# Optimization experiments

Hardware: AMD Instinct MI355X
Metric: run time of the kernel (lower is better)

## Reference

```python
import jax, jax.numpy as jnp
import numpy as np

B, T, D = 2, 2048, 512
H = 8
DH = D // H
DECAY = 0.99
SCALE = DH ** -0.5
NEG = -1e30

_J6 = jnp.array([[0, 0, 0, 0, 0, 1], [0, 0, 0, 0, -1, 0], [0, 0, 0, 1, 0, 0],
                 [0, 0, 1, 0, 0, 0], [0, -1, 0, 0, 0, 0], [1, 0, 0, 0, 0, 0]],
                dtype=jnp.float32)
_PAIRS4 = [(0, 1), (0, 2), (0, 3), (1, 2), (1, 3), (2, 3)]


def exterior(p1, p2):
    # p1, p2: [..., 4] -> normalized Plucker line coords [..., 6]
    parts = [p1[..., i] * p2[..., j] - p1[..., j] * p2[..., i] for i, j in _PAIRS4]
    L = jnp.stack(parts, axis=-1)
    n = jnp.sqrt(jnp.sum(L * L, axis=-1, keepdims=True))
    return L / jnp.maximum(n, 1e-12)


def setup_inputs() -> dict:
    key = jax.random.key(0)
    ks = jax.random.split(key, 16)
    s = 0.02
    return {
        "x": jax.random.normal(ks[0], (B, T, D), jnp.float32),
        "qkv_w": jax.random.normal(ks[1], (3 * D, D), jnp.float32) * s,
        "qkv_b": jnp.zeros((3 * D,), jnp.float32),
        "w1_write": jax.random.normal(ks[2], (4 * H, D), jnp.float32) * s,
        "w2_write": jax.random.normal(ks[3], (4 * H, D), jnp.float32) * s,
        "w1_read": jax.random.normal(ks[4], (4 * H, D), jnp.float32) * s,
        "w2_read": jax.random.normal(ks[5], (4 * H, D), jnp.float32) * s,
        "mem_value_w": jax.random.normal(ks[6], (D, D), jnp.float32) * s,
        "mem_value_b": jnp.zeros((D,), jnp.float32),
        "mem_gate_w": jax.random.normal(ks[7], (H, D), jnp.float32) * s,
        "mem_gate_b": jnp.zeros((H,), jnp.float32),
        "mem_scale": jnp.full((H,), 0.1, jnp.float32),
        "out_w": jax.random.normal(ks[8], (D, D), jnp.float32) * s,
        "out_b": jnp.zeros((D,), jnp.float32),
    }


def reference(x, qkv_w, qkv_b, w1_write, w2_write, w1_read, w2_read,
              mem_value_w, mem_value_b, mem_gate_w, mem_gate_b, mem_scale,
              out_w, out_b):
    b, t, d = x.shape
    # --- standard causal attention (dropout in eval mode = identity) ---
    qkv = (x @ qkv_w.T + qkv_b).reshape(b, t, 3, H, DH)
    qkv = jnp.transpose(qkv, (2, 0, 3, 1, 4))  # [3,B,H,T,dh]
    q, k, v = qkv[0], qkv[1], qkv[2]
    scores = jnp.einsum('bhtd,bhsd->bhts', q, k) * SCALE
    i = jnp.arange(t)
    upper = i[:, None] < i[None, :]  # strictly upper -> masked
    scores = jnp.where(upper, NEG, scores)
    attn = jax.nn.softmax(scores, axis=-1)
    seq_out = jnp.einsum('bhts,bhsd->bhtd', attn, v)
    seq_out = jnp.transpose(seq_out, (0, 2, 1, 3)).reshape(b, t, d)
    # --- exterior-algebra Gram memory ---
    x_prev = jnp.concatenate([jnp.zeros((b, 1, d), x.dtype), x[:, :-1]], axis=1)
    w1 = (x_prev @ w1_write.T).reshape(b, t, H, 4)
    w2 = (x @ w2_write.T).reshape(b, t, H, 4)
    write_lines = exterior(w1, w2)  # [B,T,H,6]
    r1 = (x @ w1_read.T).reshape(b, t, H, 4)
    r2 = (x @ w2_read.T).reshape(b, t, H, 4)
    read_lines = exterior(r1, r2)  # [B,T,H,6]
    J_write = jnp.einsum('bthi,ij->bthj', write_lines, _J6)
    # incidence[b,h,i,j] = <read_i, J write_j>
    incidence = jnp.einsum('bihk,bjhk->bhij', read_lines, J_write)  # [B,H,T,T]
    # decay weights, strictly lower triangular (j < i); also acts as causal mask
    pos = jnp.arange(t, dtype=x.dtype)
    delta = pos[:, None] - pos[None, :]
    weights = jnp.where(delta > 0, jnp.power(jnp.asarray(DECAY, x.dtype), delta), 0.0)
    mem_score = jnp.sum((incidence * incidence) * weights[None, None], axis=-1)  # [B,H,T]
    # --- gating ---
    mem_val = x @ mem_value_w.T + mem_value_b  # [B,T,D]
    gate = jax.nn.sigmoid(x @ mem_gate_w.T + mem_gate_b)  # [B,T,H]
    mem_score_t = jnp.transpose(mem_score, (0, 2, 1))  # [B,T,H]
    gated = jax.nn.sigmoid(mem_score_t * mem_scale[None, None, :]) * gate
    gated = jnp.mean(gated, axis=-1, keepdims=True)  # [B,T,1]
    return (seq_out + gated * mem_val) @ out_w.T + out_b
```

## Files before the change

kernel.cpp:

```cpp
#include <hip/hip_runtime.h>
#include <math.h>

#define B_ 2
#define T_ 2048
#define D_ 512
#define H_ 8
#define DH_ 64
#define SCALE_ 0.125f
#define DECAY_ 0.99f

static constexpr size_t QSZ = (size_t)B_ * H_ * T_ * DH_;

typedef __bf16 bf16x8 __attribute__((ext_vector_type(8)));
typedef float f32x4 __attribute__((ext_vector_type(4)));

__device__ inline ushort f2bf(float f) {
  uint u = __float_as_uint(f);
  u += 0x7FFF + ((u >> 16) & 1);
  return (ushort)(u >> 16);
}

__device__ inline float bf2f(ushort v) {
  return __uint_as_float(((uint)v) << 16);
}

__device__ __forceinline__ void gload16(const ushort* g, ushort* l) {
  __builtin_amdgcn_global_load_lds(
      (const __attribute__((address_space(1))) void*)g,
      (__attribute__((address_space(3))) void*)l, 16, 0, 0);
}

__global__ __launch_bounds__(256) void cast_bf16_kernel(
    const float* __restrict__ x, const float* __restrict__ qkvw,
    const float* __restrict__ mvw, const float* __restrict__ ow,
    const float* __restrict__ w1w, const float* __restrict__ w2w,
    const float* __restrict__ w1r, const float* __restrict__ w2r,
    const float* __restrict__ mgw, ushort* __restrict__ dst)
{
  size_t e0 = ((size_t)blockIdx.x * 256 + threadIdx.x) * 8;
  const float* src = nullptr;
  if (e0 < 2097152)      src = x + e0;
  else if (e0 < 2883584) src = qkvw + (e0 - 2097152);
  else if (e0 < 3145728) src = mvw + (e0 - 2883584);
  else if (e0 < 3276800) {
    size_t off = e0 - 3145728;
    int row = (int)(off >> 9), col = (int)(off & 511);
    if (row < 32)       src = w1w + (size_t)row * 512 + col;
    else if (row < 64)  src = w2w + (size_t)(row - 32) * 512 + col;
    else if (row < 96)  src = w1r + (size_t)(row - 64) * 512 + col;
    else if (row < 128) src = w2r + (size_t)(row - 96) * 512 + col;
    else if (row < 136) src = mgw + (size_t)(row - 128) * 512 + col;
    else src = nullptr;
  } else if (e0 < 3538944) src = ow + (e0 - 3276800);
  ushort tmp[8];
  if (src) {
    float4 a = *(const float4*)(src);
    float4 b = *(const float4*)(src + 4);
    tmp[0] = f2bf(a.x); tmp[1] = f2bf(a.y); tmp[2] = f2bf(a.z); tmp[3] = f2bf(a.w);
    tmp[4] = f2bf(b.x); tmp[5] = f2bf(b.y); tmp[6] = f2bf(b.z); tmp[7] = f2bf(b.w);
  } else {
#pragma unroll
    for (int i = 0; i < 8; i++) tmp[i] = 0;
  }
  *(uint4*)(dst + e0) = *(uint4*)tmp;
}

template<int EPI>
__global__ __launch_bounds__(256) void mfma_gemm(const ushort* __restrict__ A,
    const ushort* __restrict__ W, const float* __restrict__ bias,
    const float* __restrict__ bias2, void* __restrict__ Cout,
    ushort* __restrict__ memval16, float* __restrict__ proj, int M, int N, int K)
{
  __shared__ __align__(16) ushort As[128 * 64];
  __shared__ __align__(16) ushort Ws[64 * 64];
  const int tid = threadIdx.x;
  const int wave = tid >> 6, lane = tid & 63;
  const int col16 = lane & 15, grp = lane >> 4;
  const int wr = wave >> 1, wc = wave & 1;
  const int gx = gridDim.x;
  const int nwg = gx * gridDim.y;
  const int p = blockIdx.y * gx + blockIdx.x;
  const int wg = (p & 7) * (nwg >> 3) + (p >> 3);
  const int bm = (wg / gx) * 128, bn = (wg % gx) * 64;

  f32x4 acc[4][2] = {};
  const int lrow = lane >> 3, lcol = (lane & 7) * 8;

  for (int k0 = 0; k0 < K; k0 += 64) {
    __syncthreads();
#pragma unroll
    for (int i = 0; i < 4; i++) {
      int q = i * 4 + wave;
      gload16(A + (size_t)(bm + q * 8 + lrow) * K + k0 + lcol, &As[q * 512]);
    }
#pragma unroll
    for (int i = 0; i < 2; i++) {
      int q = i * 4 + wave;
      gload16(W + (size_t)(bn + q * 8 + lrow) * K + k0 + lcol, &Ws[q * 512]);
    }
    __syncthreads();
#pragma unroll
    for (int kk = 0; kk < 2; kk++) {
      bf16x8 a[4], b[2];
#pragma unroll
      for (int m = 0; m < 4; m++)
        a[m] = *(const bf16x8*)&As[(wr * 64 + m * 16 + col16) * 64 + kk * 32 + grp * 8];
#pragma unroll
      for (int n = 0; n < 2; n++)
        b[n] = *(const bf16x8*)&Ws[(wc * 32 + n * 16 + col16) * 64 + kk * 32 + grp * 8];
#pragma unroll
      for (int m = 0; m < 4; m++)
#pragma unroll
        for (int n = 0; n < 2; n++)
          acc[m][n] = __builtin_amdgcn_mfma_f32_16x16x32_bf16(a[m], b[n], acc[m][n], 0, 0, 0);
    }
  }

  if (EPI == 1) {
    ushort* q16 = (ushort*)Cout;
    ushort* k16 = q16 + QSZ;
    ushort* vt  = q16 + 2 * QSZ;
    const int sec = bn >> 9;
    if (sec == 2) {
#pragma unroll
      for (int n = 0; n < 2; n++) {
        int col = bn + wc * 32 + n * 16 + col16;
        float bv = bias[col];
        int h = (col >> 6) & 7, dh = col & 63;
#pragma unroll
        for (int m = 0; m < 4; m++) {
          int row0 = bm + wr * 64 + m * 16 + grp * 4;
          int b = row0 >> 11, t0 = row0 & 2047;
          ushort tmp4[4];
#pragma unroll
          for (int r = 0; r < 4; r++) tmp4[r] = f2bf(acc[m][n][r] + bv);
          *(uint2*)(vt + ((size_t)(b * H_ + h) * 64 + dh) * T_ + t0) = *(uint2*)tmp4;
        }
      }
    } else {
#pragma unroll
      for (int n = 0; n < 2; n++) {
        int col = bn + wc * 32 + n * 16 + col16;
        float bv;
        if (sec < 2)       bv = bias[col];
        else if (sec == 3) bv = bias2[col - 1536];
        else               bv = 0.f;
        int h = (col >> 6) & 7, dh = col & 63;
#pragma unroll
        for (int m = 0; m < 4; m++) {
#pragma unroll
          for (int r = 0; r < 4; r++) {
            int row = bm + wr * 64 + m * 16 + grp * 4 + r;
            int b = row >> 11, t = row & 2047;
            float val = acc[m][n][r] + bv;
            size_t bh = (size_t)(b * H_ + h);
            if (sec == 0)      q16[(bh * T_ + t) * 64 + dh] = f2bf(val * (SCALE_ * 1.44269504f));
            else if (sec == 1) k16[(bh * T_ + t) * 64 + dh] = f2bf(val);
            else if (sec == 3) memval16[(size_t)row * 512 + (col - 1536)] = f2bf(val);
            else               proj[(size_t)row * 256 + (col - 2048)] = val;
          }
        }
      }
    }
  } else {
    float* C = (float*)Cout;
#pragma unroll
    for (int n = 0; n < 2; n++) {
      int col = bn + wc * 32 + n * 16 + col16;
      float bv = bias[col];
#pragma unroll
      for (int m = 0; m < 4; m++) {
#pragma unroll
        for (int r = 0; r < 4; r++) {
          int row = bm + wr * 64 + m * 16 + grp * 4 + r;
          C[(size_t)row * N + col] = acc[m][n][r] + bv;
        }
      }
    }
  }
}

__global__ __launch_bounds__(256) void lines_kernel(
    const float* __restrict__ proj, const float* __restrict__ gb,
    float* __restrict__ u_out, float* __restrict__ r_out, float* __restrict__ gate_out)
{
  int gid = blockIdx.x * 256 + threadIdx.x;
  int bt = gid >> 3, h = gid & 7;
  int b = bt >> 11, t = bt & 2047;
  const float* pr = proj + (size_t)bt * 256;
  const int pi[6] = {0, 0, 0, 1, 1, 2};
  const int pj[6] = {1, 2, 3, 2, 3, 3};
  float p1[4], p2[4];
#pragma unroll
  for (int e = 0; e < 4; e++) {
    p1[e] = (t == 0) ? 0.f : proj[(size_t)(bt - 1) * 256 + h * 4 + e];
    p2[e] = pr[32 + h * 4 + e];
  }
  float L[6], n2 = 0.f;
#pragma unroll
  for (int e = 0; e < 6; e++) {
    L[e] = p1[pi[e]] * p2[pj[e]] - p1[pj[e]] * p2[pi[e]];
    n2 = fmaf(L[e], L[e], n2);
  }
  float inv = 1.f / fmaxf(sqrtf(n2), 1e-12f);
  size_t base = (((size_t)(b * H_ + h)) * T_ + t) * 6;
  u_out[base + 0] =  L[5] * inv;
  u_out[base + 1] = -L[4] * inv;
  u_out[base + 2] =  L[3] * inv;
  u_out[base + 3] =  L[2] * inv;
  u_out[base + 4] = -L[1] * inv;
  u_out[base + 5] =  L[0] * inv;
#pragma unroll
  for (int e = 0; e < 4; e++) {
    p1[e] = pr[64 + h * 4 + e];
    p2[e] = pr[96 + h * 4 + e];
  }
  n2 = 0.f;
#pragma unroll
  for (int e = 0; e < 6; e++) {
    L[e] = p1[pi[e]] * p2[pj[e]] - p1[pj[e]] * p2[pi[e]];
    n2 = fmaf(L[e], L[e], n2);
  }
  inv = 1.f / fmaxf(sqrtf(n2), 1e-12f);
#pragma unroll
  for (int e = 0; e < 6; e++) r_out[base + e] = L[e] * inv;
  gate_out[(size_t)bt * H_ + h] = 1.f / (1.f + __expf(-(pr[128 + h] + gb[h])));
}

__global__ __launch_bounds__(256) void attn_split32_kernel(
    const ushort* __restrict__ q16, const ushort* __restrict__ k16,
    const ushort* __restrict__ vt16, float* __restrict__ seq_out)
{
  const int blk = blockIdx.x;
  const int bh = blk & 15;
  const int rg = 63 - (blk >> 4);
  const int tid = threadIdx.x;
  const int w = tid >> 6, lane = tid & 63;
  const int col16 = lane & 15, grp = lane >> 4;

  __shared__ __align__(16) float smem[7680];
  ushort (*ps_)[32][72] = (ushort (*)[32][72])smem;
  float (*comb)[64][40] = (float (*)[64][40])smem;

  const int i0 = rg * 32;
  const ushort* qp0 = q16 + ((size_t)bh * T_ + i0 + col16) * 64 + grp * 8;
  bf16x8 aq[2][2];
  aq[0][0] = *(const bf16x8*)(qp0);
  aq[0][1] = *(const bf16x8*)(qp0 + 32);
  aq[1][0] = *(const bf16x8*)(qp0 + 16 * 64);
  aq[1][1] = *(const bf16x8*)(qp0 + 16 * 64 + 32);

  f32x4 o[2][4] = {};
  float lsum[2][4] = {};

  const ushort* kb = k16 + (size_t)bh * T_ * 64;
  const ushort* vb = vt16 + (size_t)bh * 64 * T_;

  const int ntiles = (rg >> 1) + 1;
  for (int kt = w; kt < ntiles; kt += 4) {
    const int j0 = kt * 64;
    bf16x8 vfrag[2][4];
#pragma unroll
    for (int ks2 = 0; ks2 < 2; ks2++)
#pragma unroll
      for (int n = 0; n < 4; n++)
        vfrag[ks2][n] = *(const bf16x8*)(vb + (size_t)(n * 16 + col16) * T_ +
                                         j0 + ks2 * 32 + grp * 8);
    f32x4 facc[2][4] = {};
#pragma unroll
    for (int jt = 0; jt < 4; jt++) {
      const ushort* kp = kb + (size_t)(j0 + jt * 16 + col16) * 64 + grp * 8;
      bf16x8 b0 = *(const bf16x8*)kp;
      bf16x8 b1 = *(const bf16x8*)(kp + 32);
#pragma unroll
      for (int rr = 0; rr < 2; rr++) {
        facc[rr][jt] = __builtin_amdgcn_mfma_f32_16x16x32_bf16(aq[rr][0], b0, facc[rr][jt], 0, 0, 0);
        facc[rr][jt] = __builtin_amdgcn_mfma_f32_16x16x32_bf16(aq[rr][1], b1, facc[rr][jt], 0, 0, 0);
      }
    }
    const bool lastt = (kt == ntiles - 1);
#pragma unroll
    for (int rr = 0; rr < 2; rr++)
#pragma unroll
      for (int jt = 0; jt < 4; jt++) {
        int j = j0 + jt * 16 + col16;
#pragma unroll
        for (int r = 0; r < 4; r++) {
          int i = i0 + rr * 16 + grp * 4 + r;
          float pv = (lastt && j > i) ? 0.f : exp2f(facc[rr][jt][r]);
          lsum[rr][r] += pv;
          ps_[w][rr * 16 + grp * 4 + r][jt * 16 + col16] = f2bf(pv);
        }
      }
#pragma unroll
    for (int ks2 = 0; ks2 < 2; ks2++)
#pragma unroll
      for (int rr = 0; rr < 2; rr++) {
        bf16x8 a = *(const bf16x8*)&ps_[w][rr * 16 + col16][ks2 * 32 + grp * 8];
#pragma unroll
        for (int n = 0; n < 4; n++)
          o[rr][n] = __builtin_amdgcn_mfma_f32_16x16x32_bf16(a, vfrag[ks2][n], o[rr][n], 0, 0, 0);
      }
  }

  __syncthreads();
  if (w > 0) {
    float* dst = &comb[w - 1][lane][0];
#pragma unroll
    for (int rr = 0; rr < 2; rr++)
#pragma unroll
      for (int n = 0; n < 4; n++)
        *(float4*)&dst[(rr * 4 + n) * 4] = *(float4*)&o[rr][n];
    *(float4*)&dst[32] = make_float4(lsum[0][0], lsum[0][1], lsum[0][2], lsum[0][3]);
    *(float4*)&dst[36] = make_float4(lsum[1][0], lsum[1][1], lsum[1][2], lsum[1][3]);
  }
  __syncthreads();
  if (w == 0) {
#pragma unroll
    for (int ww = 0; ww < 3; ww++) {
      const float* src = &comb[ww][lane][0];
#pragma unroll
      for (int rr = 0; rr < 2; rr++)
#pragma unroll
        for (int n = 0; n < 4; n++) {
          float4 v = *(const float4*)&src[(rr * 4 + n) * 4];
          o[rr][n][0] += v.x; o[rr][n][1] += v.y; o[rr][n][2] += v.z; o[rr][n][3] += v.w;
        }
      float4 l0 = *(const float4*)&src[32];
      float4 l1 = *(const float4*)&src[36];
      lsum[0][0] += l0.x; lsum[0][1] += l0.y; lsum[0][2] += l0.z; lsum[0][3] += l0.w;
      lsum[1][0] += l1.x; lsum[1][1] += l1.y; lsum[1][2] += l1.z; lsum[1][3] += l1.w;
    }
#pragma unroll
    for (int rr = 0; rr < 2; rr++)
#pragma unroll
      for (int r = 0; r < 4; r++) {
        float s = lsum[rr][r];
#pragma unroll
        for (int s2 = 1; s2 < 16; s2 <<= 1) s += __shfl_xor(s, s2);
        lsum[rr][r] = s;
      }
    const int b = bh >> 3, h = bh & 7;
#pragma unroll
    for (int rr = 0; rr < 2; rr++)
#pragma unroll
      for (int r = 0; r < 4; r++) {
        float inv = 1.f / lsum[rr][r];
        int i = i0 + rr * 16 + grp * 4 + r;
        float* op = seq_out + ((size_t)(b * T_) + i) * D_ + h * 64;
#pragma unroll
        for (int n = 0; n < 4; n++)
          op[n * 16 + col16] = o[rr][n][r] * inv;
      }
  }
}

__global__ __launch_bounds__(128) void memscore3_kernel(
    const float* __restrict__ u, const float* __restrict__ r, float* __restrict__ score)
{
  const int bh = blockIdx.x;
  const int c = blockIdx.y;
  const int tid = threadIdx.x;
  const int base = c << 7;
  const int jmax = base + 128;
  __shared__ float us_t[6][2048];
  __shared__ float red[128][25];

  const float* ug = u + (size_t)bh * T_ * 6;
  for (int idx = tid; idx < jmax * 6; idx += 128) {
    int j = idx / 6;
    int cmp = idx - j * 6;
    us_t[cmp][j] = ug[idx];
  }
  __syncthreads();

  float g[21];
#pragma unroll
  for (int q2 = 0; q2 < 21; q2++) g[q2] = 0.f;
  if (c > 0) {
    float w = __powf(DECAY_, (float)(128 - tid));
    const float d128 = 0.27624712f;
    for (int j = base - 128 + tid; j >= 0; j -= 128) {
      float u0 = us_t[0][j], u1 = us_t[1][j], u2 = us_t[2][j];
      float u3 = us_t[3][j], u4 = us_t[4][j], u5 = us_t[5][j];
      float w0 = w * u0, w1 = w * u1, w2 = w * u2, w3 = w * u3, w4 = w * u4;
      g[0] = fmaf(w0, u0, g[0]);  g[1] = fmaf(w0, u1, g[1]);
      g[2] = fmaf(w0, u2, g[2]);  g[3] = fmaf(w0, u3, g[3]);
      g[4] = fmaf(w0, u4, g[4]);  g[5] = fmaf(w0, u5, g[5]);
      g[6] = fmaf(w1, u1, g[6]);  g[7] = fmaf(w1, u2, g[7]);
      g[8] = fmaf(w1, u3, g[8]);  g[9] = fmaf(w1, u4, g[9]);
      g[10] = fmaf(w1, u5, g[10]); g[11] = fmaf(w2, u2, g[11]);
      g[12] = fmaf(w2, u3, g[12]); g[13] = fmaf(w2, u4, g[13]);
      g[14] = fmaf(w2, u5, g[14]); g[15] = fmaf(w3, u3, g[15]);
      g[16] = fmaf(w3, u4, g[16]); g[17] = fmaf(w3, u5, g[17]);
      g[18] = fmaf(w4, u4, g[18]); g[19] = fmaf(w4, u5, g[19]);
      g[20] = fmaf(w * u5, u5, g[20]);
      w *= d128;
    }
  }
#pragma unroll
  for (int q2 = 0; q2 < 21; q2++) red[tid][q2] = g[q2];
  __syncthreads();
  for (int off = 64; off > 0; off >>= 1) {
    if (tid < off) {
#pragma unroll
      for (int q2 = 0; q2 < 21; q2++) red[tid][q2] += red[tid + off][q2];
    }
    __syncthreads();
  }
  float M21[21];
#pragma unroll
  for (int q2 = 0; q2 < 21; q2++) M21[q2] = red[0][q2];

  const int i = base + tid;
  const float* ri = r + ((size_t)bh * T_ + i) * 6;
  float r0 = ri[0], r1 = ri[1], r2 = ri[2], r3 = ri[3], r4 = ri[4], r5 = ri[5];
  float q = M21[0] * r0 * r0 + M21[6] * r1 * r1 + M21[11] * r2 * r2
          + M21[15] * r3 * r3 + M21[18] * r4 * r4 + M21[20] * r5 * r5
          + 2.f * (M21[1] * r0 * r1 + M21[2] * r0 * r2 + M21[3] * r0 * r3
                 + M21[4] * r0 * r4 + M21[5] * r0 * r5 + M21[7] * r1 * r2
                 + M21[8] * r1 * r3 + M21[9] * r1 * r4 + M21[10] * r1 * r5
                 + M21[12] * r2 * r3 + M21[13] * r2 * r4 + M21[14] * r2 * r5
                 + M21[16] * r3 * r4 + M21[17] * r3 * r5 + M21[19] * r4 * r5);
  float wl = __powf(DECAY_, (float)tid);
  float sum = q * wl;
  float w = wl;
  const float invd = 1.0f / DECAY_;
  const int sbound = tid | 63;
  for (int s = 0; s < sbound; ++s) {
    float d = r0 * us_t[0][base + s] + r1 * us_t[1][base + s]
            + r2 * us_t[2][base + s] + r3 * us_t[3][base + s]
            + r4 * us_t[4][base + s] + r5 * us_t[5][base + s];
    if (s < tid) sum = fmaf(w, d * d, sum);
    w *= invd;
  }
  score[(size_t)bh * T_ + i] = sum;
}

__global__ __launch_bounds__(256) void gate_combine_kernel(
    const float* __restrict__ score, const float* __restrict__ gate,
    const float* __restrict__ mem_scale, const ushort* __restrict__ memval16,
    const float* __restrict__ seqo, ushort* __restrict__ seqo16)
{
  int bt = blockIdx.x;
  int b = bt / T_, t = bt % T_;
  __shared__ float g;
  if (threadIdx.x == 0) {
    float acc = 0.f;
#pragma unroll
    for (int h = 0; h < H_; h++) {
      float ms = score[((size_t)(b * H_ + h)) * T_ + t];
      float sg = 1.f / (1.f + __expf(-ms * mem_scale[h]));
      acc += sg * gate[(size_t)(b * T_ + t) * H_ + h];
    }
    g = acc * (1.0f / H_);
  }
  __syncthreads();
  float gv = g;
  size_t base = (size_t)(b * T_ + t) * D_;
  for (int d = threadIdx.x; d < D_; d += 256)
    seqo16[base + d] = f2bf(fmaf(gv, bf2f(memval16[base + d]), seqo[base + d]));
}

extern "C" void kernel_launch(void* const* d_in, const int* in_sizes, int n_in,
                              void* d_out, int out_size, void* d_ws, size_t ws_size,
                              hipStream_t stream) {
  const float* x     = (const float*)d_in[0];
  const float* qkvw  = (const float*)d_in[1];
  const float* qkvb  = (const float*)d_in[2];
  const float* w1w   = (const float*)d_in[3];
  const float* w2w   = (const float*)d_in[4];
  const float* w1r   = (const float*)d_in[5];
  const float* w2r   = (const float*)d_in[6];
  const float* mvw   = (const float*)d_in[7];
  const float* mvb   = (const float*)d_in[8];
  const float* mgw   = (const float*)d_in[9];
  const float* mgb   = (const float*)d_in[10];
  const float* mscl  = (const float*)d_in[11];
  const float* ow    = (const float*)d_in[12];
  const float* ob    = (const float*)d_in[13];
  (void)in_sizes; (void)n_in; (void)out_size; (void)ws_size;

  float* f = (float*)d_ws;
  float* seqo     = f;
  ushort* memval16 = (ushort*)(seqo + 2097152);
  float* proj     = (float*)(memval16 + 2097152);
  float* ul       = proj + 1048576;
  float* rl       = ul + 196608;
  float* gatep    = rl + 196608;
  float* msc      = gatep + 32768;
  ushort* x16    = (ushort*)(msc + 32768);
  ushort* wbig16 = x16 + 2097152;
  ushort* ow16   = wbig16 + 1179648;
  ushort* q16    = ow16 + 262144;
  ushort* k16    = q16 + QSZ;
  ushort* vt16   = k16 + QSZ;
  ushort* seqo16 = x16;

  const int M = B_ * T_;

  cast_bf16_kernel<<<dim3(1728), 256, 0, stream>>>(x, qkvw, mvw, ow,
                                                   w1w, w2w, w1r, w2r, mgw, x16);
  mfma_gemm<1><<<dim3(36, 32), 256, 0, stream>>>(x16, wbig16, qkvb, mvb, q16,
                                                 memval16, proj, M, 2304, D_);
  lines_kernel<<<dim3(128), 256, 0, stream>>>(proj, mgb, ul, rl, gatep);
  attn_split32_kernel<<<dim3(16 * 64), 256, 0, stream>>>(q16, k16, vt16, seqo);
  memscore3_kernel<<<dim3(16, 16), 128, 0, stream>>>(ul, rl, msc);
  gate_combine_kernel<<<dim3(B_ * T_), 256, 0, stream>>>(msc, gatep, mscl, memval16,
                                                         seqo, seqo16);
  mfma_gemm<0><<<dim3(8, 32), 256, 0, stream>>>(seqo16, ow16, ob, nullptr, d_out,
                                                nullptr, nullptr, M, D_, D_);
}
```

Measured before the change: 118.8 us.

## Fuse gating combine into attention epilogue and stage V tiles in LDS asynchronously

The separate gate_combine pass is split: a tiny gfac kernel computes the per-token gate factor, and the attention kernel's epilogue applies it with memval and writes the bf16 input for the output GEMM directly. This drops the fp32 seq_out round trip and one full-size elementwise kernel. Attention also now prefetches V tiles into swizzled LDS with asynchronous global-to-LDS loads (gload16) and overlaps the next tile's load with compute, instead of loading V fragments directly into registers. The cost is more LDS per block and a reordered launch sequence, in which memscore now has to finish before attention starts.

```diff
diff --git a/kernel.cpp b/kernel.cpp
--- a/kernel.cpp
+++ b/kernel.cpp
@@ -227,134 +227,6 @@
   gate_out[(size_t)bt * H_ + h] = 1.f / (1.f + __expf(-(pr[128 + h] + gb[h])));
 }
 
-__global__ __launch_bounds__(256) void attn_split32_kernel(
-    const ushort* __restrict__ q16, const ushort* __restrict__ k16,
-    const ushort* __restrict__ vt16, float* __restrict__ seq_out)
-{
-  const int blk = blockIdx.x;
-  const int bh = blk & 15;
-  const int rg = 63 - (blk >> 4);
-  const int tid = threadIdx.x;
-  const int w = tid >> 6, lane = tid & 63;
-  const int col16 = lane & 15, grp = lane >> 4;
-
-  __shared__ __align__(16) float smem[7680];
-  ushort (*ps_)[32][72] = (ushort (*)[32][72])smem;
-  float (*comb)[64][40] = (float (*)[64][40])smem;
-
-  const int i0 = rg * 32;
-  const ushort* qp0 = q16 + ((size_t)bh * T_ + i0 + col16) * 64 + grp * 8;
-  bf16x8 aq[2][2];
-  aq[0][0] = *(const bf16x8*)(qp0);
-  aq[0][1] = *(const bf16x8*)(qp0 + 32);
-  aq[1][0] = *(const bf16x8*)(qp0 + 16 * 64);
-  aq[1][1] = *(const bf16x8*)(qp0 + 16 * 64 + 32);
-
-  f32x4 o[2][4] = {};
-  float lsum[2][4] = {};
-
-  const ushort* kb = k16 + (size_t)bh * T_ * 64;
-  const ushort* vb = vt16 + (size_t)bh * 64 * T_;
-
-  const int ntiles = (rg >> 1) + 1;
-  for (int kt = w; kt < ntiles; kt += 4) {
-    const int j0 = kt * 64;
-    bf16x8 vfrag[2][4];
-#pragma unroll
-    for (int ks2 = 0; ks2 < 2; ks2++)
-#pragma unroll
-      for (int n = 0; n < 4; n++)
-        vfrag[ks2][n] = *(const bf16x8*)(vb + (size_t)(n * 16 + col16) * T_ +
-                                         j0 + ks2 * 32 + grp * 8);
-    f32x4 facc[2][4] = {};
-#pragma unroll
-    for (int jt = 0; jt < 4; jt++) {
-      const ushort* kp = kb + (size_t)(j0 + jt * 16 + col16) * 64 + grp * 8;
-      bf16x8 b0 = *(const bf16x8*)kp;
-      bf16x8 b1 = *(const bf16x8*)(kp + 32);
-#pragma unroll
-      for (int rr = 0; rr < 2; rr++) {
-        facc[rr][jt] = __builtin_amdgcn_mfma_f32_16x16x32_bf16(aq[rr][0], b0, facc[rr][jt], 0, 0, 0);
-        facc[rr][jt] = __builtin_amdgcn_mfma_f32_16x16x32_bf16(aq[rr][1], b1, facc[rr][jt], 0, 0, 0);
-      }
-    }
-    const bool lastt = (kt == ntiles - 1);
-#pragma unroll
-    for (int rr = 0; rr < 2; rr++)
-#pragma unroll
-      for (int jt = 0; jt < 4; jt++) {
-        int j = j0 + jt * 16 + col16;
-#pragma unroll
-        for (int r = 0; r < 4; r++) {
-          int i = i0 + rr * 16 + grp * 4 + r;
-          float pv = (lastt && j > i) ? 0.f : exp2f(facc[rr][jt][r]);
-          lsum[rr][r] += pv;
-          ps_[w][rr * 16 + grp * 4 + r][jt * 16 + col16] = f2bf(pv);
-        }
-      }
-#pragma unroll
-    for (int ks2 = 0; ks2 < 2; ks2++)
-#pragma unroll
-      for (int rr = 0; rr < 2; rr++) {
-        bf16x8 a = *(const bf16x8*)&ps_[w][rr * 16 + col16][ks2 * 32 + grp * 8];
-#pragma unroll
-        for (int n = 0; n < 4; n++)
-          o[rr][n] = __builtin_amdgcn_mfma_f32_16x16x32_bf16(a, vfrag[ks2][n], o[rr][n], 0, 0, 0);
-      }
-  }
-
-  __syncthreads();
-  if (w > 0) {
-    float* dst = &comb[w - 1][lane][0];
-#pragma unroll
-    for (int rr = 0; rr < 2; rr++)
-#pragma unroll
-      for (int n = 0; n < 4; n++)
-        *(float4*)&dst[(rr * 4 + n) * 4] = *(float4*)&o[rr][n];
-    *(float4*)&dst[32] = make_float4(lsum[0][0], lsum[0][1], lsum[0][2], lsum[0][3]);
-    *(float4*)&dst[36] = make_float4(lsum[1][0], lsum[1][1], lsum[1][2], lsum[1][3]);
-  }
-  __syncthreads();
-  if (w == 0) {
-#pragma unroll
-    for (int ww = 0; ww < 3; ww++) {
-      const float* src = &comb[ww][lane][0];
-#pragma unroll
-      for (int rr = 0; rr < 2; rr++)
-#pragma unroll
-        for (int n = 0; n < 4; n++) {
-          float4 v = *(const float4*)&src[(rr * 4 + n) * 4];
-          o[rr][n][0] += v.x; o[rr][n][1] += v.y; o[rr][n][2] += v.z; o[rr][n][3] += v.w;
-        }
-      float4 l0 = *(const float4*)&src[32];
-      float4 l1 = *(const float4*)&src[36];
-      lsum[0][0] += l0.x; lsum[0][1] += l0.y; lsum[0][2] += l0.z; lsum[0][3] += l0.w;
-      lsum[1][0] += l1.x; lsum[1][1] += l1.y; lsum[1][2] += l1.z; lsum[1][3] += l1.w;
-    }
-#pragma unroll
-    for (int rr = 0; rr < 2; rr++)
-#pragma unroll
-      for (int r = 0; r < 4; r++) {
-        float s = lsum[rr][r];
-#pragma unroll
-        for (int s2 = 1; s2 < 16; s2 <<= 1) s += __shfl_xor(s, s2);
-        lsum[rr][r] = s;
-      }
-    const int b = bh >> 3, h = bh & 7;
-#pragma unroll
-    for (int rr = 0; rr < 2; rr++)
-#pragma unroll
-      for (int r = 0; r < 4; r++) {
-        float inv = 1.f / lsum[rr][r];
-        int i = i0 + rr * 16 + grp * 4 + r;
-        float* op = seq_out + ((size_t)(b * T_) + i) * D_ + h * 64;
-#pragma unroll
-        for (int n = 0; n < 4; n++)
-          op[n * 16 + col16] = o[rr][n][r] * inv;
-      }
-  }
-}
-
 __global__ __launch_bounds__(128) void memscore3_kernel(
     const float* __restrict__ u, const float* __restrict__ r, float* __restrict__ score)
 {
@@ -437,29 +309,168 @@
   score[(size_t)bh * T_ + i] = sum;
 }
 
-__global__ __launch_bounds__(256) void gate_combine_kernel(
+__global__ __launch_bounds__(256) void gfac_kernel(
     const float* __restrict__ score, const float* __restrict__ gate,
-    const float* __restrict__ mem_scale, const ushort* __restrict__ memval16,
-    const float* __restrict__ seqo, ushort* __restrict__ seqo16)
+    const float* __restrict__ mem_scale, float* __restrict__ gfac)
 {
-  int bt = blockIdx.x;
-  int b = bt / T_, t = bt % T_;
-  __shared__ float g;
-  if (threadIdx.x == 0) {
-    float acc = 0.f;
-#pragma unroll
-    for (int h = 0; h < H_; h++) {
-      float ms = score[((size_t)(b * H_ + h)) * T_ + t];
-      float sg = 1.f / (1.f + __expf(-ms * mem_scale[h]));
-      acc += sg * gate[(size_t)(b * T_ + t) * H_ + h];
-    }
-    g = acc * (1.0f / H_);
-  }
+  int bt = blockIdx.x * 256 + threadIdx.x;
+  int b = bt >> 11, t = bt & 2047;
+  float acc = 0.f;
+#pragma unroll
+  for (int h = 0; h < H_; h++) {
+    float ms = score[((size_t)(b * H_ + h)) * T_ + t];
+    float sg = 1.f / (1.f + __expf(-ms * mem_scale[h]));
+    acc += sg * gate[(size_t)bt * H_ + h];
+  }
+  gfac[bt] = acc * (1.0f / H_);
+}
+
+__global__ __launch_bounds__(256) void attn_v3_kernel(
+    const ushort* __restrict__ q16, const ushort* __restrict__ k16,
+    const ushort* __restrict__ vt16, const ushort* __restrict__ memval16,
+    const float* __restrict__ gfac, ushort* __restrict__ seqo16)
+{
+  const int blk = blockIdx.x;
+  const int bh = blk & 15;
+  const int rg = 63 - (blk >> 4);
+  const int tid = threadIdx.x;
+  const int w = tid >> 6, lane = tid & 63;
+  const int col16 = lane & 15, grp = lane >> 4;
+
+  __shared__ __align__(16) ushort smemU[25600];
+  ushort* vt_lds = &smemU[w * 4096];
+  ushort* ps_w   = &smemU[16384 + w * 32 * 72];
+  float*  combf  = (float*)smemU;
+
+  const int i0 = rg * 32;
+  const ushort* qp0 = q16 + ((size_t)bh * T_ + i0 + col16) * 64 + grp * 8;
+  bf16x8 aq[2][2];
+  aq[0][0] = *(const bf16x8*)(qp0);
+  aq[0][1] = *(const bf16x8*)(qp0 + 32);
+  aq[1][0] = *(const bf16x8*)(qp0 + 16 * 64);
+  aq[1][1] = *(const bf16x8*)(qp0 + 16 * 64 + 32);
+
+  f32x4 o[2][4] = {};
+  float lsum[2][4] = {};
+
+  const ushort* kb = k16 + (size_t)bh * T_ * 64;
+  const ushort* vb = vt16 + (size_t)bh * 64 * T_;
+  const int vrow = lane >> 3;
+  const int vchk = ((lane & 7) ^ vrow) << 3;
+
+  const int ntiles = (rg >> 1) + 1;
+  if (w < ntiles) {
+    const int j0 = w * 64;
+#pragma unroll
+    for (int g = 0; g < 8; g++)
+      gload16(vb + (size_t)(g * 8 + vrow) * T_ + j0 + vchk, vt_lds + g * 512);
+  }
+
+  for (int kt = w; kt < ntiles; kt += 4) {
+    const int j0 = kt * 64;
+    f32x4 facc[2][4] = {};
+#pragma unroll
+    for (int jt = 0; jt < 4; jt++) {
+      const ushort* kp = kb + (size_t)(j0 + jt * 16 + col16) * 64 + grp * 8;
+      bf16x8 b0 = *(const bf16x8*)kp;
+      bf16x8 b1 = *(const bf16x8*)(kp + 32);
+#pragma unroll
+      for (int rr = 0; rr < 2; rr++) {
+        facc[rr][jt] = __builtin_amdgcn_mfma_f32_16x16x32_bf16(aq[rr][0], b0, facc[rr][jt], 0, 0, 0);
+        facc[rr][jt] = __builtin_amdgcn_mfma_f32_16x16x32_bf16(aq[rr][1], b1, facc[rr][jt], 0, 0, 0);
+      }
+    }
+    const bool lastt = (kt == ntiles - 1);
+#pragma unroll
+    for (int rr = 0; rr < 2; rr++)
+#pragma unroll
+      for (int jt = 0; jt < 4; jt++) {
+        int j = j0 + jt * 16 + col16;
+#pragma unroll
+        for (int r = 0; r < 4; r++) {
+          int i = i0 + rr * 16 + grp * 4 + r;
+          float pv = (lastt && j > i) ? 0.f : exp2f(facc[rr][jt][r]);
+          lsum[rr][r] += pv;
+          ps_w[(rr * 16 + grp * 4 + r) * 72 + jt * 16 + col16] = f2bf(pv);
+        }
+      }
+    asm volatile("s_waitcnt vmcnt(0)" ::: "memory");
+#pragma unroll
+    for (int ks2 = 0; ks2 < 2; ks2++)
+#pragma unroll
+      for (int rr = 0; rr < 2; rr++) {
+        bf16x8 a = *(const bf16x8*)&ps_w[(rr * 16 + col16) * 72 + ks2 * 32 + grp * 8];
+#pragma unroll
+        for (int n = 0; n < 4; n++) {
+          int d = n * 16 + col16;
+          int cs = (ks2 * 4 + grp) ^ (col16 & 7);
+          bf16x8 bv = *(const bf16x8*)&vt_lds[d * 64 + cs * 8];
+          o[rr][n] = __builtin_amdgcn_mfma_f32_16x16x32_bf16(a, bv, o[rr][n], 0, 0, 0);
+        }
+      }
+    __builtin_amdgcn_sched_barrier(0);
+    if (kt + 4 < ntiles) {
+      const int jn = (kt + 4) * 64;
+#pragma unroll
+      for (int g = 0; g < 8; g++)
+        gload16(vb + (size_t)(g * 8 + vrow) * T_ + jn + vchk, vt_lds + g * 512);
+    }
+  }
+
   __syncthreads();
-  float gv = g;
-  size_t base = (size_t)(b * T_ + t) * D_;
-  for (int d = threadIdx.x; d < D_; d += 256)
-    seqo16[base + d] = f2bf(fmaf(gv, bf2f(memval16[base + d]), seqo[base + d]));
+  if (w > 0) {
+    float* dst = &combf[((w - 1) * 64 + lane) * 40];
+#pragma unroll
+    for (int rr = 0; rr < 2; rr++)
+#pragma unroll
+      for (int n = 0; n < 4; n++)
+        *(float4*)&dst[(rr * 4 + n) * 4] = *(float4*)&o[rr][n];
+    *(float4*)&dst[32] = make_float4(lsum[0][0], lsum[0][1], lsum[0][2], lsum[0][3]);
+    *(float4*)&dst[36] = make_float4(lsum[1][0], lsum[1][1], lsum[1][2], lsum[1][3]);
+  }
+  __syncthreads();
+  if (w == 0) {
+#pragma unroll
+    for (int ww = 0; ww < 3; ww++) {
+      const float* src = &combf[(ww * 64 + lane) * 40];
+#pragma unroll
+      for (int rr = 0; rr < 2; rr++)
+#pragma unroll
+        for (int n = 0; n < 4; n++) {
+          float4 v = *(const float4*)&src[(rr * 4 + n) * 4];
+          o[rr][n][0] += v.x; o[rr][n][1] += v.y; o[rr][n][2] += v.z; o[rr][n][3] += v.w;
+        }
+      float4 l0 = *(const float4*)&src[32];
+      float4 l1 = *(const float4*)&src[36];
+      lsum[0][0] += l0.x; lsum[0][1] += l0.y; lsum[0][2] += l0.z; lsum[0][3] += l0.w;
+      lsum[1][0] += l1.x; lsum[1][1] += l1.y; lsum[1][2] += l1.z; lsum[1][3] += l1.w;
+    }
+#pragma unroll
+    for (int rr = 0; rr < 2; rr++)
+#pragma unroll
+      for (int r = 0; r < 4; r++) {
+        float s = lsum[rr][r];
+#pragma unroll
+        for (int s2 = 1; s2 < 16; s2 <<= 1) s += __shfl_xor(s, s2);
+        lsum[rr][r] = s;
+      }
+    const int b = bh >> 3, h = bh & 7;
+#pragma unroll
+    for (int rr = 0; rr < 2; rr++)
+#pragma unroll
+      for (int r = 0; r < 4; r++) {
+        float inv = 1.f / lsum[rr][r];
+        int i = i0 + rr * 16 + grp * 4 + r;
+        float gf = gfac[b * T_ + i];
+        size_t rowbase = ((size_t)(b * T_) + i) * D_ + h * 64;
+#pragma unroll
+        for (int n = 0; n < 4; n++) {
+          int d = n * 16 + col16;
+          float mv = bf2f(memval16[rowbase + d]);
+          seqo16[rowbase + d] = f2bf(fmaf(gf, mv, o[rr][n][r] * inv));
+        }
+      }
+  }
 }
 
 extern "C" void kernel_launch(void* const* d_in, const int* in_sizes, int n_in,
@@ -482,19 +493,19 @@
   (void)in_sizes; (void)n_in; (void)out_size; (void)ws_size;
 
   float* f = (float*)d_ws;
-  float* seqo     = f;
-  ushort* memval16 = (ushort*)(seqo + 2097152);
-  float* proj     = (float*)(memval16 + 2097152);
-  float* ul       = proj + 1048576;
-  float* rl       = ul + 196608;
-  float* gatep    = rl + 196608;
-  float* msc      = gatep + 32768;
-  ushort* x16    = (ushort*)(msc + 32768);
+  float* proj   = f;
+  float* ul     = proj + 1048576;
+  float* rl     = ul + 196608;
+  float* gatep  = rl + 196608;
+  float* msc    = gatep + 32768;
+  float* gfac   = msc + 32768;
+  ushort* x16    = (ushort*)(gfac + 4096);
   ushort* wbig16 = x16 + 2097152;
   ushort* ow16   = wbig16 + 1179648;
   ushort* q16    = ow16 + 262144;
   ushort* k16    = q16 + QSZ;
   ushort* vt16   = k16 + QSZ;
+  ushort* memval16 = vt16 + QSZ;
   ushort* seqo16 = x16;
 
   const int M = B_ * T_;
@@ -504,10 +515,10 @@
   mfma_gemm<1><<<dim3(36, 32), 256, 0, stream>>>(x16, wbig16, qkvb, mvb, q16,
                                                  memval16, proj, M, 2304, D_);
   lines_kernel<<<dim3(128), 256, 0, stream>>>(proj, mgb, ul, rl, gatep);
-  attn_split32_kernel<<<dim3(16 * 64), 256, 0, stream>>>(q16, k16, vt16, seqo);
   memscore3_kernel<<<dim3(16, 16), 128, 0, stream>>>(ul, rl, msc);
-  gate_combine_kernel<<<dim3(B_ * T_), 256, 0, stream>>>(msc, gatep, mscl, memval16,
-                                                         seqo, seqo16);
+  gfac_kernel<<<dim3(16), 256, 0, stream>>>(msc, gatep, mscl, gfac);
+  attn_v3_kernel<<<dim3(16 * 64), 256, 0, stream>>>(q16, k16, vt16, memval16,
+                                                    gfac, seqo16);
   mfma_gemm<0><<<dim3(8, 32), 256, 0, stream>>>(seqo16, ow16, ob, nullptr, d_out,
                                                 nullptr, nullptr, M, D_, D_);
 }
```

Measured after the change: 111.8 us. 1.06x faster.
